# Kernel optimization log

Hardware: AMD Instinct MI355X
Metric: run time of the kernel (lower is better)

## Reference

```python
import jax, jax.numpy as jnp
import numpy as np

B, S, D = 4, 2048, 1024
H, DH = 16, 64  # d_model = H*DH = 1024
NEG = 1e10


def setup_inputs() -> dict:
    key = jax.random.key(0)
    ks = jax.random.split(key, 5)
    scale = 1.0 / np.sqrt(D)
    x = jax.random.normal(ks[0], (B, S, D), dtype=jnp.float32)
    mask = jax.random.randint(ks[1], (B, S), 0, 2).astype(jnp.float32)
    Wq = jax.random.normal(ks[2], (D, H * DH), dtype=jnp.float32) * scale
    Wk = jax.random.normal(ks[3], (D, H * DH), dtype=jnp.float32) * scale
    Wv = jax.random.normal(ks[4], (D, H * DH), dtype=jnp.float32) * scale
    z = jnp.zeros((H * DH,), dtype=jnp.float32)
    return {"x": x, "mask": mask, "Wq": Wq, "bq": z, "Wk": Wk, "bk": z,
            "Wv": Wv, "bv": z}


def reference(x, mask, Wq, bq, Wk, bk, Wv, bv):
    # projections -> [B, H, S, DH]
    def proj(W, b):
        y = x @ W + b
        return y.reshape(B, S, H, DH).transpose(0, 2, 1, 3)

    q, k, v = proj(Wq, bq), proj(Wk, bk), proj(Wv, bv)
    scores = jnp.einsum("bhsd,bhtd->bhst", q, k) / np.sqrt(DH)
    m = mask[:, None, None, :]                      # [B,1,1,S]
    scores = scores - (1.0 - m) * NEG               # additive mask
    probs = jax.nn.softmax(scores, axis=-1)         # stable (max-subtract)
    probs = probs * m                               # multiplicative mask
    out = jnp.einsum("bhst,bhtd->bhsd", probs, v)   # [B,H,S,DH]
    return out.transpose(0, 2, 1, 3).reshape(B, S, H * DH)
```

## Files before the change

### kernel.cpp

```cpp
#include <hip/hip_runtime.h>

typedef float f32x4 __attribute__((ext_vector_type(4)));
typedef float f32x16 __attribute__((ext_vector_type(16)));
typedef _Float16 f16;
typedef _Float16 f16x2 __attribute__((ext_vector_type(2)));
typedef _Float16 f16x8 __attribute__((ext_vector_type(8)));
typedef unsigned int u32x2 __attribute__((ext_vector_type(2)));
typedef unsigned short u16;
typedef unsigned short u16x4 __attribute__((ext_vector_type(4)));
typedef unsigned int u32;

#define S_LEN 2048
#define NHEAD 16
#define DHEAD 64
#define DMODEL 1024
#define NBATCH 4

__device__ __forceinline__ void gload16(const u16* g, const uint4* l) {
  __builtin_amdgcn_global_load_lds((const __attribute__((address_space(1))) void*)g,
                                   (__attribute__((address_space(3))) void*)l, 16, 0, 0);
}


__global__ void cvt_x(const float* __restrict__ x, u16* __restrict__ o, int n4) {
  int i = blockIdx.x * blockDim.x + threadIdx.x;
  int st = gridDim.x * blockDim.x;
  for (; i < n4; i += st) {
    float4 v = reinterpret_cast<const float4*>(x)[i];
    uint2 r;
    r.x = __builtin_bit_cast(u32, __builtin_amdgcn_cvt_pkrtz(v.x, v.y));
    r.y = __builtin_bit_cast(u32, __builtin_amdgcn_cvt_pkrtz(v.z, v.w));
    reinterpret_cast<uint2*>(o)[i] = r;
  }
}

__global__ void trans_w(const float* __restrict__ W, u16* __restrict__ wt) {
  __shared__ float t[32][33];
  int bx = blockIdx.x * 32, by = blockIdx.y * 32;
  int tx = threadIdx.x & 31, ty = threadIdx.x >> 5;
#pragma unroll
  for (int i = 0; i < 32; i += 8)
    t[ty + i][tx] = W[(size_t)(by + ty + i) * DMODEL + bx + tx];
  __syncthreads();
#pragma unroll
  for (int i = 0; i < 32; i += 8)
    wt[(size_t)(bx + ty + i) * DMODEL + by + tx] = __builtin_bit_cast(u16, (f16)t[tx][ty + i]);
}

__global__ __launch_bounds__(256) void qkv_gemm(
    const u16* __restrict__ A, const u16* __restrict__ Wt,
    const float* __restrict__ bq, const float* __restrict__ bk, const float* __restrict__ bv,
    const float* __restrict__ mask,
    u16* __restrict__ Qo, u16* __restrict__ Ko, u16* __restrict__ Vo)
{
  __shared__ uint4 As4[3][512];
  __shared__ uint4 Bs4[3][512];
  const int tid = threadIdx.x;
  const int lane = tid & 63;
  const int wid = tid >> 6;
  const int l31 = lane & 31, hi = lane >> 5;
  const int m0 = blockIdx.x * 128;
  const int n0 = blockIdx.y * 128;
  const int wr = (wid >> 1) * 64, wc = (wid & 1) * 64;

  f32x16 acc[2][2] = {};

  const int c0 = wid * 64 + lane, c1 = c0 + 256;
  const int r0 = c0 >> 2, r1 = c1 >> 2;
  const int p4 = lane & 3;
  const int sl0 = p4 ^ ((r0 >> 1) & 3);
  const int sl1 = p4 ^ ((r1 >> 1) & 3);
  const u16* ag0 = A  + (size_t)(m0 + r0) * 1024 + sl0 * 8;
  const u16* ag1 = A  + (size_t)(m0 + r1) * 1024 + sl1 * 8;
  const u16* bg0 = Wt + (size_t)(n0 + r0) * 1024 + sl0 * 8;
  const u16* bg1 = Wt + (size_t)(n0 + r1) * 1024 + sl1 * 8;

  auto stage = [&](int buf, int kt) {
    gload16(ag0 + kt, &As4[buf][wid * 64]);
    gload16(ag1 + kt, &As4[buf][wid * 64 + 256]);
    gload16(bg0 + kt, &Bs4[buf][wid * 64]);
    gload16(bg1 + kt, &Bs4[buf][wid * 64 + 256]);
  };

  int aoff[2][2], boff[2][2];
#pragma unroll
  for (int mi = 0; mi < 2; mi++) {
    int r = wr + mi * 32 + l31;
#pragma unroll
    for (int ks = 0; ks < 2; ks++)
      aoff[mi][ks] = r * 32 + (((ks * 2 + hi) ^ ((r >> 1) & 3)) * 8);
  }
#pragma unroll
  for (int ni = 0; ni < 2; ni++) {
    int r = wc + ni * 32 + l31;
#pragma unroll
    for (int ks = 0; ks < 2; ks++)
      boff[ni][ks] = r * 32 + (((ks * 2 + hi) ^ ((r >> 1) & 3)) * 8);
  }

  stage(0, 0);
  stage(1, 32);
  __syncthreads();

  const int NT = 1024 / 32;
  for (int it = 0; it < NT; ++it) {
    if (it + 1 < NT) asm volatile("s_waitcnt vmcnt(4)" ::: "memory");
    else             asm volatile("s_waitcnt vmcnt(0)" ::: "memory");
    __builtin_amdgcn_s_barrier();
    __builtin_amdgcn_sched_barrier(0);
    const int cur = it % 3;
    if (it + 2 < NT) stage((it + 2) % 3, (it + 2) * 32);

    const u16* As = (const u16*)&As4[cur][0];
    const u16* Bs = (const u16*)&Bs4[cur][0];
    f16x8 af[2][2], bf[2][2];
#pragma unroll
    for (int mi = 0; mi < 2; mi++)
#pragma unroll
      for (int ks = 0; ks < 2; ks++)
        af[mi][ks] = *(const f16x8*)&As[aoff[mi][ks]];
#pragma unroll
    for (int ni = 0; ni < 2; ni++)
#pragma unroll
      for (int ks = 0; ks < 2; ks++)
        bf[ni][ks] = *(const f16x8*)&Bs[boff[ni][ks]];

#pragma unroll
    for (int ks = 0; ks < 2; ks++)
#pragma unroll
      for (int mi = 0; mi < 2; mi++)
#pragma unroll
        for (int ni = 0; ni < 2; ni++)
          acc[mi][ni] = __builtin_amdgcn_mfma_f32_32x32x16_f16(af[mi][ks], bf[ni][ks], acc[mi][ni], 0, 0, 0);
  }

  const int sel = n0 >> 10;
  const float* bias = (sel == 0) ? bq : (sel == 1) ? bk : bv;
  const int nbase = (n0 & 1023) + wc;
  const float QSCALE = 0.18033688011112042f;
#pragma unroll
  for (int mi = 0; mi < 2; mi++)
#pragma unroll
    for (int ni = 0; ni < 2; ni++) {
      const int ncol = nbase + ni * 32 + l31;
      const float bi = bias[ncol];
      const int h = ncol >> 6, dh = ncol & 63;
#pragma unroll
      for (int r4 = 0; r4 < 4; r4++) {
        const int rowb = m0 + wr + mi * 32 + 8 * r4 + 4 * hi;
        const int bb = rowb >> 11, s0 = rowb & 2047;
        const size_t bh = (size_t)(bb * NHEAD + h);
        if (sel == 0) {
#pragma unroll
          for (int j = 0; j < 4; j++)
            Qo[(bh * S_LEN + s0 + j) * DHEAD + dh] =
                __builtin_bit_cast(u16, (f16)((acc[mi][ni][r4 * 4 + j] + bi) * QSCALE));
        } else if (sel == 1) {
#pragma unroll
          for (int j = 0; j < 4; j++)
            Ko[(bh * S_LEN + s0 + j) * DHEAD + dh] =
                __builtin_bit_cast(u16, (f16)(acc[mi][ni][r4 * 4 + j] + bi));
        } else {
          const float4 mk = *(const float4*)&mask[bb * S_LEN + s0];
          u16x4 pk;
#pragma unroll
          for (int j = 0; j < 4; j++) {
            float v = acc[mi][ni][r4 * 4 + j] + bi;
            float mj = (j == 0) ? mk.x : (j == 1) ? mk.y : (j == 2) ? mk.z : mk.w;
            if (mj <= 0.f) v = 0.f;
            pk[j] = __builtin_bit_cast(u16, (f16)v);
          }
          *(u16x4*)&Vo[(bh * DHEAD + dh) * S_LEN + s0] = pk;
        }
      }
    }
}

__global__ __launch_bounds__(256, 2) void attn(
    const u16* __restrict__ Q, const u16* __restrict__ K, const u16* __restrict__ Vt,
    const float* __restrict__ mask, float* __restrict__ out)
{
  __shared__ uint4 Ks4[3][512];
  __shared__ uint4 Vs4[3][512];
  __shared__ __align__(16) u16 MsAll[S_LEN];
  const int tid = threadIdx.x;
  const int lane = tid & 63, wid = tid >> 6;
  const int l31 = lane & 31, hi = lane >> 5;
  const int sid = blockIdx.x;
  const int qt = (sid >> 3) & 7;
  const int bh = (sid & 7) + 8 * (sid >> 6);
  const int b = bh >> 4, h = bh & 15;
  const size_t base = (size_t)bh * S_LEN * DHEAD;
  const u16* Qp = Q + base;
  const u16* Kp = K + base;
  const u16* Vp = Vt + base;
  const float* mp = mask + b * S_LEN;
  const int q0 = qt * 256 + wid * 64;

  f16x8 aqA[4], aqB[4];
#pragma unroll
  for (int kc = 0; kc < 4; kc++) {
    aqA[kc] = *(const f16x8*)&Qp[(size_t)(q0 + l31) * DHEAD + kc * 16 + hi * 8];
    aqB[kc] = *(const f16x8*)&Qp[(size_t)(q0 + 32 + l31) * DHEAD + kc * 16 + hi * 8];
  }

  f32x16 accO0A = {}, accO1A = {}, accLA = {};
  f32x16 accO0B = {}, accO1B = {}, accLB = {};

  const int cA_ = wid * 128 + lane, cB_ = cA_ + 64;
  const int rk0 = cA_ >> 3, rk1 = cB_ >> 3;
  const int p8 = lane & 7;
  const int cc0 = (p8 - ((rk0 + (rk0 >> 3)) & 7)) & 7;
  const int cc1 = (p8 - ((rk1 + (rk1 >> 3)) & 7)) & 7;
  const u16* kg0 = Kp + (size_t)rk0 * DHEAD + cc0 * 8;
  const u16* kg1 = Kp + (size_t)rk1 * DHEAD + cc1 * 8;
  const u16* vg0 = Vp + (size_t)rk0 * S_LEN + cc0 * 8;
  const u16* vg1 = Vp + (size_t)rk1 * S_LEN + cc1 * 8;

  auto stage = [&](int buf) {
    gload16(kg0, &Ks4[buf][wid * 128]); gload16(kg1, &Ks4[buf][wid * 128 + 64]);
    gload16(vg0, &Vs4[buf][wid * 128]); gload16(vg1, &Vs4[buf][wid * 128 + 64]);
    kg0 += 64 * DHEAD; kg1 += 64 * DHEAD; vg0 += 64; vg1 += 64;
  };

  const int swA = (l31 + (l31 >> 3)) & 7;
  const int swB = (swA + 4) & 7;
  int idxA[4], idxB[4];
#pragma unroll
  for (int kc = 0; kc < 4; kc++) {
    idxA[kc] = l31 * 8 + ((kc * 2 + hi + swA) & 7);
    idxB[kc] = (32 + l31) * 8 + ((kc * 2 + hi + swB) & 7);
  }

  {
    float4 ml0 = *(const float4*)&mp[tid * 8];
    float4 ml1 = *(const float4*)&mp[tid * 8 + 4];
    uint4 w;
    w.x = __builtin_bit_cast(u32, __builtin_amdgcn_cvt_pkrtz(ml0.x, ml0.y));
    w.y = __builtin_bit_cast(u32, __builtin_amdgcn_cvt_pkrtz(ml0.z, ml0.w));
    w.z = __builtin_bit_cast(u32, __builtin_amdgcn_cvt_pkrtz(ml1.x, ml1.y));
    w.w = __builtin_bit_cast(u32, __builtin_amdgcn_cvt_pkrtz(ml1.z, ml1.w));
    *(uint4*)&MsAll[tid * 8] = w;
  }
  stage(0);
  stage(1);
  __syncthreads();

  const int NT = S_LEN / 64;
  for (int it = 0; it < NT; ++it) {
    if (it + 1 < NT) asm volatile("s_waitcnt vmcnt(4)" ::: "memory");
    else             asm volatile("s_waitcnt vmcnt(0)" ::: "memory");
    __builtin_amdgcn_s_barrier();
    __builtin_amdgcn_sched_barrier(0);
    const int cur = it % 3;
    const uint4* ks = &Ks4[cur][0];
    const uint4* vs = &Vs4[cur][0];
    if (it + 2 < NT) stage((it + 2) % 3);

    f32x16 sA0 = {}, sA1 = {}, sB0 = {}, sB1 = {};
    __builtin_amdgcn_s_setprio(1);
#pragma unroll
    for (int kc = 0; kc < 4; kc++) {
      f16x8 k0 = *(const f16x8*)&ks[idxA[kc]];
      f16x8 k1 = *(const f16x8*)&ks[idxB[kc]];
      sA0 = __builtin_amdgcn_mfma_f32_32x32x16_f16(k0, aqA[kc], sA0, 0, 0, 0);
      sA1 = __builtin_amdgcn_mfma_f32_32x32x16_f16(k1, aqA[kc], sA1, 0, 0, 0);
      sB0 = __builtin_amdgcn_mfma_f32_32x32x16_f16(k0, aqB[kc], sB0, 0, 0, 0);
      sB1 = __builtin_amdgcn_mfma_f32_32x32x16_f16(k1, aqB[kc], sB1, 0, 0, 0);
    }
    __builtin_amdgcn_s_setprio(0);

#pragma unroll
    for (int g = 0; g < 4; g++) {
      const f32x16& srcA = (g < 2) ? sA0 : sA1;
      const f32x16& srcB = (g < 2) ? sB0 : sB1;
      const int o = (g & 1) * 8;
      u32 wa[4], wb[4];
#pragma unroll
      for (int s = 0; s < 4; s++) {
        wa[s] = __builtin_bit_cast(u32, __builtin_amdgcn_cvt_pkrtz(
                    __builtin_amdgcn_exp2f(srcA[o + 2 * s]),
                    __builtin_amdgcn_exp2f(srcA[o + 2 * s + 1])));
        wb[s] = __builtin_bit_cast(u32, __builtin_amdgcn_cvt_pkrtz(
                    __builtin_amdgcn_exp2f(srcB[o + 2 * s]),
                    __builtin_amdgcn_exp2f(srcB[o + 2 * s + 1])));
      }
      u32x2 rA0 = __builtin_amdgcn_permlane32_swap(wa[0], wa[2], false, false);
      u32x2 rA1 = __builtin_amdgcn_permlane32_swap(wa[1], wa[3], false, false);
      u32x2 rB0 = __builtin_amdgcn_permlane32_swap(wb[0], wb[2], false, false);
      u32x2 rB1 = __builtin_amdgcn_permlane32_swap(wb[1], wb[3], false, false);
      uint4 f4A; f4A.x = rA0[0]; f4A.y = rA1[0]; f4A.z = rA0[1]; f4A.w = rA1[1];
      uint4 f4B; f4B.x = rB0[0]; f4B.y = rB1[0]; f4B.z = rB0[1]; f4B.w = rB1[1];
      f16x8 fA = __builtin_bit_cast(f16x8, f4A);
      f16x8 fB = __builtin_bit_cast(f16x8, f4B);
      f16x8 bv0 = *(const f16x8*)&vs[idxA[g]];
      f16x8 bv1 = *(const f16x8*)&vs[idxB[g]];
      f16x8 bm = *(const f16x8*)&MsAll[it * 64 + g * 16 + hi * 8];
      __builtin_amdgcn_s_setprio(1);
      accO0A = __builtin_amdgcn_mfma_f32_32x32x16_f16(fA, bv0, accO0A, 0, 0, 0);
      accO1A = __builtin_amdgcn_mfma_f32_32x32x16_f16(fA, bv1, accO1A, 0, 0, 0);
      accLA  = __builtin_amdgcn_mfma_f32_32x32x16_f16(fA, bm,  accLA,  0, 0, 0);
      accO0B = __builtin_amdgcn_mfma_f32_32x32x16_f16(fB, bv0, accO0B, 0, 0, 0);
      accO1B = __builtin_amdgcn_mfma_f32_32x32x16_f16(fB, bv1, accO1B, 0, 0, 0);
      accLB  = __builtin_amdgcn_mfma_f32_32x32x16_f16(fB, bm,  accLB,  0, 0, 0);
      __builtin_amdgcn_s_setprio(0);
    }
  }

#pragma unroll
  for (int r = 0; r < 16; r++) {
    int qr = (r & 3) + 8 * (r >> 2) + 4 * hi;
    float lA = accLA[r], lB = accLB[r];
    float iA = (lA > 0.f) ? 1.f / lA : 0.f;
    float iB = (lB > 0.f) ? 1.f / lB : 0.f;
    float* opA = out + ((size_t)(b * S_LEN + q0 + qr) * DMODEL) + h * DHEAD;
    float* opB = out + ((size_t)(b * S_LEN + q0 + 32 + qr) * DMODEL) + h * DHEAD;
    opA[l31] = accO0A[r] * iA;
    opA[32 + l31] = accO1A[r] * iA;
    opB[l31] = accO0B[r] * iB;
    opB[32 + l31] = accO1B[r] * iB;
  }
}

extern "C" void kernel_launch(void* const* d_in, const int* in_sizes, int n_in,
                              void* d_out, int out_size, void* d_ws, size_t ws_size,
                              hipStream_t stream) {
  const float* x    = (const float*)d_in[0];
  const float* mask = (const float*)d_in[1];
  const float* Wq   = (const float*)d_in[2];
  const float* bq   = (const float*)d_in[3];
  const float* Wk   = (const float*)d_in[4];
  const float* bk   = (const float*)d_in[5];
  const float* Wv   = (const float*)d_in[6];
  const float* bv   = (const float*)d_in[7];
  float* out = (float*)d_out;

  u16* xb = (u16*)d_ws;
  u16* wt = xb + (size_t)8192 * 1024;
  u16* Qb = wt + (size_t)3072 * 1024;
  u16* Kb = Qb + (size_t)8388608;
  u16* Vb = Kb + (size_t)8388608;

  cvt_x<<<2048, 256, 0, stream>>>(x, xb, (8192 * 1024) / 4);
  trans_w<<<dim3(32, 32), 256, 0, stream>>>(Wq, wt);
  trans_w<<<dim3(32, 32), 256, 0, stream>>>(Wk, wt + (size_t)1024 * 1024);
  trans_w<<<dim3(32, 32), 256, 0, stream>>>(Wv, wt + (size_t)2 * 1024 * 1024);
  qkv_gemm<<<dim3(64, 24), 256, 0, stream>>>(xb, wt, bq, bk, bv, mask, Qb, Kb, Vb);
  attn<<<512, 256, 0, stream>>>(Qb, Kb, Vb, mask, out);
}
```

Before: 168.7 us.

## Halve attention query tile per wave and double grid for higher occupancy

Each wave now handles 32 query rows instead of 64, so per-thread accumulators and Q fragments are halved. Launch bounds move to 4 blocks per SM and the grid doubles to 1024 blocks. The K/V ring buffer drops from triple to double buffering with a full vmcnt(0) wait each iteration, which cuts LDS use. In exchange each K/V tile is reused by half as many query rows, so K/V traffic doubles, and the shallower prefetch exposes more load latency, which the extra occupancy is meant to hide.

```diff
diff --git a/kernel.cpp b/kernel.cpp
--- a/kernel.cpp
+++ b/kernel.cpp
@@ -176,36 +176,33 @@
     }
 }
 
-__global__ __launch_bounds__(256, 2) void attn(
+__global__ __launch_bounds__(256, 4) void attn(
     const u16* __restrict__ Q, const u16* __restrict__ K, const u16* __restrict__ Vt,
     const float* __restrict__ mask, float* __restrict__ out)
 {
-  __shared__ uint4 Ks4[3][512];
-  __shared__ uint4 Vs4[3][512];
+  __shared__ uint4 Ks4[2][512];
+  __shared__ uint4 Vs4[2][512];
   __shared__ __align__(16) u16 MsAll[S_LEN];
   const int tid = threadIdx.x;
   const int lane = tid & 63, wid = tid >> 6;
   const int l31 = lane & 31, hi = lane >> 5;
   const int sid = blockIdx.x;
-  const int qt = (sid >> 3) & 7;
-  const int bh = (sid & 7) + 8 * (sid >> 6);
+  const int qt = (sid >> 3) & 15;
+  const int bh = (sid & 7) + 8 * (sid >> 7);
   const int b = bh >> 4, h = bh & 15;
   const size_t base = (size_t)bh * S_LEN * DHEAD;
   const u16* Qp = Q + base;
   const u16* Kp = K + base;
   const u16* Vp = Vt + base;
   const float* mp = mask + b * S_LEN;
-  const int q0 = qt * 256 + wid * 64;
-
-  f16x8 aqA[4], aqB[4];
-#pragma unroll
-  for (int kc = 0; kc < 4; kc++) {
+  const int q0 = qt * 128 + wid * 32;
+
+  f16x8 aqA[4];
+#pragma unroll
+  for (int kc = 0; kc < 4; kc++)
     aqA[kc] = *(const f16x8*)&Qp[(size_t)(q0 + l31) * DHEAD + kc * 16 + hi * 8];
-    aqB[kc] = *(const f16x8*)&Qp[(size_t)(q0 + 32 + l31) * DHEAD + kc * 16 + hi * 8];
-  }
 
   f32x16 accO0A = {}, accO1A = {}, accLA = {};
-  f32x16 accO0B = {}, accO1B = {}, accLB = {};
 
   const int cA_ = wid * 128 + lane, cB_ = cA_ + 64;
   const int rk0 = cA_ >> 3, rk1 = cB_ >> 3;
@@ -243,21 +240,19 @@
     *(uint4*)&MsAll[tid * 8] = w;
   }
   stage(0);
-  stage(1);
   __syncthreads();
 
   const int NT = S_LEN / 64;
   for (int it = 0; it < NT; ++it) {
-    if (it + 1 < NT) asm volatile("s_waitcnt vmcnt(4)" ::: "memory");
-    else             asm volatile("s_waitcnt vmcnt(0)" ::: "memory");
+    asm volatile("s_waitcnt vmcnt(0)" ::: "memory");
     __builtin_amdgcn_s_barrier();
     __builtin_amdgcn_sched_barrier(0);
-    const int cur = it % 3;
+    const int cur = it & 1;
     const uint4* ks = &Ks4[cur][0];
     const uint4* vs = &Vs4[cur][0];
-    if (it + 2 < NT) stage((it + 2) % 3);
-
-    f32x16 sA0 = {}, sA1 = {}, sB0 = {}, sB1 = {};
+    if (it + 1 < NT) stage((it + 1) & 1);
+
+    f32x16 sA0 = {}, sA1 = {};
     __builtin_amdgcn_s_setprio(1);
 #pragma unroll
     for (int kc = 0; kc < 4; kc++) {
@@ -265,34 +260,24 @@
       f16x8 k1 = *(const f16x8*)&ks[idxB[kc]];
       sA0 = __builtin_amdgcn_mfma_f32_32x32x16_f16(k0, aqA[kc], sA0, 0, 0, 0);
       sA1 = __builtin_amdgcn_mfma_f32_32x32x16_f16(k1, aqA[kc], sA1, 0, 0, 0);
-      sB0 = __builtin_amdgcn_mfma_f32_32x32x16_f16(k0, aqB[kc], sB0, 0, 0, 0);
-      sB1 = __builtin_amdgcn_mfma_f32_32x32x16_f16(k1, aqB[kc], sB1, 0, 0, 0);
     }
     __builtin_amdgcn_s_setprio(0);
 
 #pragma unroll
     for (int g = 0; g < 4; g++) {
       const f32x16& srcA = (g < 2) ? sA0 : sA1;
-      const f32x16& srcB = (g < 2) ? sB0 : sB1;
       const int o = (g & 1) * 8;
-      u32 wa[4], wb[4];
+      u32 wa[4];
 #pragma unroll
       for (int s = 0; s < 4; s++) {
         wa[s] = __builtin_bit_cast(u32, __builtin_amdgcn_cvt_pkrtz(
                     __builtin_amdgcn_exp2f(srcA[o + 2 * s]),
                     __builtin_amdgcn_exp2f(srcA[o + 2 * s + 1])));
-        wb[s] = __builtin_bit_cast(u32, __builtin_amdgcn_cvt_pkrtz(
-                    __builtin_amdgcn_exp2f(srcB[o + 2 * s]),
-                    __builtin_amdgcn_exp2f(srcB[o + 2 * s + 1])));
       }
       u32x2 rA0 = __builtin_amdgcn_permlane32_swap(wa[0], wa[2], false, false);
       u32x2 rA1 = __builtin_amdgcn_permlane32_swap(wa[1], wa[3], false, false);
-      u32x2 rB0 = __builtin_amdgcn_permlane32_swap(wb[0], wb[2], false, false);
-      u32x2 rB1 = __builtin_amdgcn_permlane32_swap(wb[1], wb[3], false, false);
       uint4 f4A; f4A.x = rA0[0]; f4A.y = rA1[0]; f4A.z = rA0[1]; f4A.w = rA1[1];
-      uint4 f4B; f4B.x = rB0[0]; f4B.y = rB1[0]; f4B.z = rB0[1]; f4B.w = rB1[1];
       f16x8 fA = __builtin_bit_cast(f16x8, f4A);
-      f16x8 fB = __builtin_bit_cast(f16x8, f4B);
       f16x8 bv0 = *(const f16x8*)&vs[idxA[g]];
       f16x8 bv1 = *(const f16x8*)&vs[idxB[g]];
       f16x8 bm = *(const f16x8*)&MsAll[it * 64 + g * 16 + hi * 8];
@@ -300,9 +285,6 @@
       accO0A = __builtin_amdgcn_mfma_f32_32x32x16_f16(fA, bv0, accO0A, 0, 0, 0);
       accO1A = __builtin_amdgcn_mfma_f32_32x32x16_f16(fA, bv1, accO1A, 0, 0, 0);
       accLA  = __builtin_amdgcn_mfma_f32_32x32x16_f16(fA, bm,  accLA,  0, 0, 0);
-      accO0B = __builtin_amdgcn_mfma_f32_32x32x16_f16(fB, bv0, accO0B, 0, 0, 0);
-      accO1B = __builtin_amdgcn_mfma_f32_32x32x16_f16(fB, bv1, accO1B, 0, 0, 0);
-      accLB  = __builtin_amdgcn_mfma_f32_32x32x16_f16(fB, bm,  accLB,  0, 0, 0);
       __builtin_amdgcn_s_setprio(0);
     }
   }
@@ -310,15 +292,11 @@
 #pragma unroll
   for (int r = 0; r < 16; r++) {
     int qr = (r & 3) + 8 * (r >> 2) + 4 * hi;
-    float lA = accLA[r], lB = accLB[r];
+    float lA = accLA[r];
     float iA = (lA > 0.f) ? 1.f / lA : 0.f;
-    float iB = (lB > 0.f) ? 1.f / lB : 0.f;
     float* opA = out + ((size_t)(b * S_LEN + q0 + qr) * DMODEL) + h * DHEAD;
-    float* opB = out + ((size_t)(b * S_LEN + q0 + 32 + qr) * DMODEL) + h * DHEAD;
     opA[l31] = accO0A[r] * iA;
     opA[32 + l31] = accO1A[r] * iA;
-    opB[l31] = accO0B[r] * iB;
-    opB[32 + l31] = accO1B[r] * iB;
   }
 }
 
@@ -346,5 +324,5 @@
   trans_w<<<dim3(32, 32), 256, 0, stream>>>(Wk, wt + (size_t)1024 * 1024);
   trans_w<<<dim3(32, 32), 256, 0, stream>>>(Wv, wt + (size_t)2 * 1024 * 1024);
   qkv_gemm<<<dim3(64, 24), 256, 0, stream>>>(xb, wt, bq, bk, bv, mask, Qb, Kb, Vb);
-  attn<<<512, 256, 0, stream>>>(Qb, Kb, Vb, mask, out);
-}
+  attn<<<1024, 256, 0, stream>>>(Qb, Kb, Vb, mask, out);
+}
```

After: 174.2 us. +3.3%, slower.

## Fold mask into score bias and sum softmax denominator in registers

Applied to the files above, without the earlier changes.

Replaces the extra MFMA that computed the masked row sum (P times mask vector) with a per-key additive bias, -1e5 for masked keys, preloaded into the score accumulators. The denominator is then accumulated directly from the exp2 values in registers and reduced across the lane halves with a shuffle, with ds_bpermute redistributing the inverse to the output rows. This removes two of six PV-phase MFMAs per group and one LDS read, in exchange for extra VALU adds, a bias load per tile, and a permuted layout for the bias array. Correctness relies on exp2 of the biased score underflowing to zero for masked keys and on the bias index permutation matching the accumulator layout.

```diff
diff --git a/kernel.cpp b/kernel.cpp
--- a/kernel.cpp
+++ b/kernel.cpp
@@ -182,7 +182,7 @@
 {
   __shared__ uint4 Ks4[3][512];
   __shared__ uint4 Vs4[3][512];
-  __shared__ __align__(16) u16 MsAll[S_LEN];
+  __shared__ float Mbias[S_LEN];
   const int tid = threadIdx.x;
   const int lane = tid & 63, wid = tid >> 6;
   const int l31 = lane & 31, hi = lane >> 5;
@@ -204,8 +204,9 @@
     aqB[kc] = *(const f16x8*)&Qp[(size_t)(q0 + 32 + l31) * DHEAD + kc * 16 + hi * 8];
   }
 
-  f32x16 accO0A = {}, accO1A = {}, accLA = {};
-  f32x16 accO0B = {}, accO1B = {}, accLB = {};
+  f32x16 accO0A = {}, accO1A = {};
+  f32x16 accO0B = {}, accO1B = {};
+  float lA = 0.f, lB = 0.f;
 
   const int cA_ = wid * 128 + lane, cB_ = cA_ + 64;
   const int rk0 = cA_ >> 3, rk1 = cB_ >> 3;
@@ -235,12 +236,14 @@
   {
     float4 ml0 = *(const float4*)&mp[tid * 8];
     float4 ml1 = *(const float4*)&mp[tid * 8 + 4];
-    uint4 w;
-    w.x = __builtin_bit_cast(u32, __builtin_amdgcn_cvt_pkrtz(ml0.x, ml0.y));
-    w.y = __builtin_bit_cast(u32, __builtin_amdgcn_cvt_pkrtz(ml0.z, ml0.w));
-    w.z = __builtin_bit_cast(u32, __builtin_amdgcn_cvt_pkrtz(ml1.x, ml1.y));
-    w.w = __builtin_bit_cast(u32, __builtin_amdgcn_cvt_pkrtz(ml1.z, ml1.w));
-    *(uint4*)&MsAll[tid * 8] = w;
+    float mv[8] = {ml0.x, ml0.y, ml0.z, ml0.w, ml1.x, ml1.y, ml1.z, ml1.w};
+#pragma unroll
+    for (int j = 0; j < 8; j++) {
+      int t = tid * 8 + j;
+      int w = t & 31, sub = (t >> 5) & 1;
+      int hi_ = (w >> 2) & 1, r_ = (w & 3) + 4 * (w >> 3);
+      Mbias[(t >> 6) * 64 + sub * 32 + hi_ * 16 + r_] = (mv[j] > 0.f) ? 0.f : -1.0e5f;
+    }
   }
   stage(0);
   stage(1);
@@ -257,7 +260,19 @@
     const uint4* vs = &Vs4[cur][0];
     if (it + 2 < NT) stage((it + 2) % 3);
 
-    f32x16 sA0 = {}, sA1 = {}, sB0 = {}, sB1 = {};
+    f32x16 ini0, ini1;
+    {
+      const f32x4* b0 = (const f32x4*)&Mbias[it * 64 + hi * 16];
+      const f32x4* b1 = (const f32x4*)&Mbias[it * 64 + 32 + hi * 16];
+#pragma unroll
+      for (int c = 0; c < 4; c++) {
+        f32x4 v0 = b0[c], v1 = b1[c];
+#pragma unroll
+        for (int j = 0; j < 4; j++) { ini0[c * 4 + j] = v0[j]; ini1[c * 4 + j] = v1[j]; }
+      }
+    }
+
+    f32x16 sA0 = ini0, sA1 = ini1, sB0 = ini0, sB1 = ini1;
     __builtin_amdgcn_s_setprio(1);
 #pragma unroll
     for (int kc = 0; kc < 4; kc++) {
@@ -278,12 +293,14 @@
       u32 wa[4], wb[4];
 #pragma unroll
       for (int s = 0; s < 4; s++) {
-        wa[s] = __builtin_bit_cast(u32, __builtin_amdgcn_cvt_pkrtz(
-                    __builtin_amdgcn_exp2f(srcA[o + 2 * s]),
-                    __builtin_amdgcn_exp2f(srcA[o + 2 * s + 1])));
-        wb[s] = __builtin_bit_cast(u32, __builtin_amdgcn_cvt_pkrtz(
-                    __builtin_amdgcn_exp2f(srcB[o + 2 * s]),
-                    __builtin_amdgcn_exp2f(srcB[o + 2 * s + 1])));
+        float ea0 = __builtin_amdgcn_exp2f(srcA[o + 2 * s]);
+        float ea1 = __builtin_amdgcn_exp2f(srcA[o + 2 * s + 1]);
+        float eb0 = __builtin_amdgcn_exp2f(srcB[o + 2 * s]);
+        float eb1 = __builtin_amdgcn_exp2f(srcB[o + 2 * s + 1]);
+        wa[s] = __builtin_bit_cast(u32, __builtin_amdgcn_cvt_pkrtz(ea0, ea1));
+        wb[s] = __builtin_bit_cast(u32, __builtin_amdgcn_cvt_pkrtz(eb0, eb1));
+        lA += ea0 + ea1;
+        lB += eb0 + eb1;
       }
       u32x2 rA0 = __builtin_amdgcn_permlane32_swap(wa[0], wa[2], false, false);
       u32x2 rA1 = __builtin_amdgcn_permlane32_swap(wa[1], wa[3], false, false);
@@ -295,24 +312,26 @@
       f16x8 fB = __builtin_bit_cast(f16x8, f4B);
       f16x8 bv0 = *(const f16x8*)&vs[idxA[g]];
       f16x8 bv1 = *(const f16x8*)&vs[idxB[g]];
-      f16x8 bm = *(const f16x8*)&MsAll[it * 64 + g * 16 + hi * 8];
       __builtin_amdgcn_s_setprio(1);
       accO0A = __builtin_amdgcn_mfma_f32_32x32x16_f16(fA, bv0, accO0A, 0, 0, 0);
       accO1A = __builtin_amdgcn_mfma_f32_32x32x16_f16(fA, bv1, accO1A, 0, 0, 0);
-      accLA  = __builtin_amdgcn_mfma_f32_32x32x16_f16(fA, bm,  accLA,  0, 0, 0);
       accO0B = __builtin_amdgcn_mfma_f32_32x32x16_f16(fB, bv0, accO0B, 0, 0, 0);
       accO1B = __builtin_amdgcn_mfma_f32_32x32x16_f16(fB, bv1, accO1B, 0, 0, 0);
-      accLB  = __builtin_amdgcn_mfma_f32_32x32x16_f16(fB, bm,  accLB,  0, 0, 0);
       __builtin_amdgcn_s_setprio(0);
     }
   }
 
+  float lAf = lA + __shfl_xor(lA, 32, 64);
+  float lBf = lB + __shfl_xor(lB, 32, 64);
+  float invA = (lAf > 0.f) ? 1.f / lAf : 0.f;
+  float invB = (lBf > 0.f) ? 1.f / lBf : 0.f;
 #pragma unroll
   for (int r = 0; r < 16; r++) {
     int qr = (r & 3) + 8 * (r >> 2) + 4 * hi;
-    float lA = accLA[r], lB = accLB[r];
-    float iA = (lA > 0.f) ? 1.f / lA : 0.f;
-    float iB = (lB > 0.f) ? 1.f / lB : 0.f;
+    float iA = __builtin_bit_cast(float,
+        (u32)__builtin_amdgcn_ds_bpermute(qr << 2, (int)__builtin_bit_cast(u32, invA)));
+    float iB = __builtin_bit_cast(float,
+        (u32)__builtin_amdgcn_ds_bpermute(qr << 2, (int)__builtin_bit_cast(u32, invB)));
     float* opA = out + ((size_t)(b * S_LEN + q0 + qr) * DMODEL) + h * DHEAD;
     float* opB = out + ((size_t)(b * S_LEN + q0 + 32 + qr) * DMODEL) + h * DHEAD;
     opA[l31] = accO0A[r] * iA;
```

Result: no change. 167.5 us (-0.7%).
